# Performance work log

Measured on AMD Instinct MI355X. Metric: run time of the kernel, lower is better.

The kernel has to match this reference:

```python
import jax, jax.numpy as jnp
import numpy as np

B, T, P, H, D = 8, 16, 14, 16, 64
L = P * P            # 196 patches (CLS excluded)
DM = H * D           # 1024 = d_model
NS = 16              # n_synos
T2 = T * T           # 256 = n_frames**2


def _conv2d(x, w, b):
    # x: [N,C,H,W], w: [O,I,kh,kw], stride 1, SAME padding (ksize//2 for odd k)
    y = jax.lax.conv_general_dilated(x, w, (1, 1), 'SAME',
                                     dimension_numbers=('NCHW', 'OIHW', 'NCHW'))
    return y + b[None, :, None, None]


def _layernorm(x, g, b):
    m = x.mean(-1, keepdims=True)
    v = x.var(-1, keepdims=True)
    return (x - m) / jnp.sqrt(v + 1e-5) * g + b


def setup_inputs() -> dict:
    key = jax.random.key(0)
    ks = jax.random.split(key, 12)
    q = jax.random.normal(ks[0], (B, T, L + 1, H, D), jnp.float32)
    k = jax.random.normal(ks[1], (B, T, L + 1, H, D), jnp.float32)
    v = jax.random.normal(ks[2], (B, T, L + 1, H, D), jnp.float32)
    syno_emb = jax.random.normal(ks[3], (NS, DM), jnp.float32) * 0.02
    t_conv_w = jax.random.normal(ks[4], (1, 2 * H, 3, 3), jnp.float32) * 0.001
    t_conv_b = jnp.zeros((1,), jnp.float32)
    ln_g = jnp.ones((T2,), jnp.float32)
    ln_b = jnp.zeros((T2,), jnp.float32)
    w1 = jax.random.normal(ks[5], (T2, T2), jnp.float32) * 0.02
    b1 = jnp.zeros((T2,), jnp.float32)
    w2 = jax.random.normal(ks[6], (T2, T2), jnp.float32) * 0.02
    b2 = jnp.zeros((T2,), jnp.float32)
    p_conv_w = jax.random.normal(ks[7], (1, T2, 3, 3), jnp.float32) * 0.001
    p_conv_b = jnp.zeros((1,), jnp.float32)
    return dict(q=q, k=k, v=v, syno_emb=syno_emb,
                t_conv_w=t_conv_w, t_conv_b=t_conv_b,
                ln_g=ln_g, ln_b=ln_b, w1=w1, b1=b1, w2=w2, b2=b2,
                p_conv_w=p_conv_w, p_conv_b=p_conv_b)


def reference(q, k, v, syno_emb, t_conv_w, t_conv_b, ln_g, ln_b,
              w1, b1, w2, b2, p_conv_w, p_conv_b):
    # ---------------- temporal detection ----------------
    def head_aff(a):  # a: [B,T,L,H,D] -> [B*L, H, T, T]
        a = a.transpose(0, 2, 1, 3, 4)  # [B,L,T,H,D]
        scale = 1.0 / (a.shape[-1] ** 0.5)
        aff = jnp.einsum('nlqhc,nlkhc->nlqkh', a * scale, a)  # [B,L,T,T,H]
        aff = jax.nn.softmax(aff, axis=-2)  # softmax over key frames
        return aff.reshape(B * L, T, T, H).transpose(0, 3, 1, 2)

    affs = jnp.concatenate([head_aff(q[:, :, 1:]), head_aff(k[:, :, 1:])],
                           axis=1)                      # [B*L, 2H, T, T]
    aff = _conv2d(affs, t_conv_w, t_conv_b)             # [B*L, 1, T, T]
    aff = aff.reshape(B, P, P, T2)                      # [B, P, P, T^2]
    h = _layernorm(aff, ln_g, ln_b)
    h = h @ w1.T + b1
    h = jax.nn.gelu(h, approximate=False)               # torch nn.GELU default
    h = h @ w2.T + b2
    aff = aff + h
    aff = aff.transpose(0, 3, 1, 2)                     # [B, T^2, P, P]
    aff = _conv2d(aff, p_conv_w, p_conv_b)              # [B, 1, P, P]
    y_t = aff.reshape(B, -1)                            # [B, P*P]

    # ---------------- spatial detection ----------------
    kf = k[:, :, 1:].reshape(B, T, L, DM)
    vf = v[:, :, 1:].reshape(B, T, L, DM)
    s_scale = 1.0 / (DM ** 0.5)
    s_aff = jnp.einsum('qw,ntkw->ntqk', syno_emb * s_scale, kf)  # [B,T,NS,L]
    s_aff = jax.nn.softmax(s_aff, axis=-1)
    s_mix = jnp.einsum('ntql,ntlw->ntqw', s_aff, vf)    # [B,T,NS,DM]
    y_s = s_mix.reshape(B, T * NS, DM).mean(axis=1)     # [B, DM]

    return (y_t, y_s)
```

## Files before the change

kernel.cpp:

```cpp
#include <hip/hip_runtime.h>
#include <hip/hip_bf16.h>
#include <math.h>

#define BB 8
#define TT 16
#define PP 14
#define LL 196
#define HH 16
#define DD 64
#define DM 1024
#define NS 16
#define T2 256
#define LP1 197

using bf16x8 = __attribute__((ext_vector_type(8))) short;
using f32x4  = __attribute__((ext_vector_type(4))) float;

__device__ __forceinline__ float dot4(float4 a, float4 b) {
    return a.x*b.x + a.y*b.y + a.z*b.z + a.w*b.w;
}

__device__ __forceinline__ uint32_t pkbf(float lo, float hi) {
    uint32_t a = __builtin_bit_cast(uint32_t, lo);
    uint32_t b = __builtin_bit_cast(uint32_t, hi);
    a += 0x7FFFu + ((a >> 16) & 1u);
    b += 0x7FFFu + ((b >> 16) & 1u);
    return (a >> 16) | (b & 0xFFFF0000u);
}

__device__ __forceinline__ void split2(float x, float y, uint32_t* h, uint32_t* lo) {
    const uint32_t hh = pkbf(x, y);
    const float hx = __builtin_bit_cast(float, hh << 16);
    const float hy = __builtin_bit_cast(float, hh & 0xFFFF0000u);
    *h = hh;
    *lo = pkbf(x - hx, y - hy);
}

__device__ __forceinline__ void pksplit(float4 p, float4 q, bf16x8& hi, bf16x8& lo) {
    uint32_t uh[4], ul[4];
    split2(p.x, p.y, &uh[0], &ul[0]);
    split2(p.z, p.w, &uh[1], &ul[1]);
    split2(q.x, q.y, &uh[2], &ul[2]);
    split2(q.z, q.w, &uh[3], &ul[3]);
    struct U4 { uint32_t v[4]; } th, tl;
    th.v[0] = uh[0]; th.v[1] = uh[1]; th.v[2] = uh[2]; th.v[3] = uh[3];
    tl.v[0] = ul[0]; tl.v[1] = ul[1]; tl.v[2] = ul[2]; tl.v[3] = ul[3];
    hi = __builtin_bit_cast(bf16x8, th);
    lo = __builtin_bit_cast(bf16x8, tl);
}

__global__ __launch_bounds__(256) void kprep(
        const float* __restrict__ syno,
        uint32_t* __restrict__ synoHi, uint32_t* __restrict__ synoLo) {
    const int i = blockIdx.x * 256 + threadIdx.x;
    const float x = syno[2 * i], y = syno[2 * i + 1];
    uint32_t h, lo;
    split2(x, y, &h, &lo);
    synoHi[i] = h;
    synoLo[i] = lo;
}

__global__ __launch_bounds__(256) void k1_temporal(
        const float* __restrict__ qin, const float* __restrict__ kin,
        const float* __restrict__ tw,  const float* __restrict__ tbv,
        const uint32_t* __restrict__ synoHi, const uint32_t* __restrict__ synoLo,
        float* __restrict__ affRaw, float* __restrict__ SLout) {
    __shared__ __align__(16) float lds_c[16 * 260];
    __shared__ __align__(16) float sl_part[4][16][16];

    const int bid = blockIdx.x, b = bid / LL, l = bid % LL;
    const int tid = threadIdx.x, wid = tid >> 6, lane = tid & 63;
    const int mrow = lane & 15;
    const int g = lane >> 4;
    const int colb = lane & 15;
    const int oq = tid >> 4, ok = tid & 15;

    const size_t rowbase = ((size_t)(b*TT + mrow)*LP1 + 1 + l)*DM + g*8;
    f32x4 acc_sl = {0.f, 0.f, 0.f, 0.f};
    float accv = tbv[0];

    float4 A[2][4];
    uint4  S[2][4];

#define K1_LOAD(BUF, IT) do {                                                  \
        const int ch_ = 2*wid + 8*((IT) >> 1) + ((IT) & 1);                    \
        const float* sp_ = ((IT) < 4) ? qin : kin;                             \
        const float* base_ = sp_ + rowbase + (size_t)(ch_ & 15) * DD;          \
        A[BUF][0] = *reinterpret_cast<const float4*>(base_);                   \
        A[BUF][1] = *reinterpret_cast<const float4*>(base_ + 4);               \
        A[BUF][2] = *reinterpret_cast<const float4*>(base_ + 32);              \
        A[BUF][3] = *reinterpret_cast<const float4*>(base_ + 36);              \
        if ((IT) >= 4) {                                                       \
            const int off_ = colb * 512 + (ch_ - 16) * 32 + g * 4;             \
            S[BUF][0] = *reinterpret_cast<const uint4*>(synoHi + off_);        \
            S[BUF][1] = *reinterpret_cast<const uint4*>(synoLo + off_);        \
            S[BUF][2] = *reinterpret_cast<const uint4*>(synoHi + off_ + 16);   \
            S[BUF][3] = *reinterpret_cast<const uint4*>(synoLo + off_ + 16);   \
        }                                                                      \
    } while (0)

#define K1_COMP(BUF, IT) do {                                                  \
        bf16x8 h1, l1, h2, l2;                                                 \
        pksplit(A[BUF][0], A[BUF][1], h1, l1);                                 \
        pksplit(A[BUF][2], A[BUF][3], h2, l2);                                 \
        f32x4 acc = {0.f, 0.f, 0.f, 0.f};                                      \
        acc = __builtin_amdgcn_mfma_f32_16x16x32_bf16(h1, h1, acc, 0, 0, 0);   \
        acc = __builtin_amdgcn_mfma_f32_16x16x32_bf16(h1, l1, acc, 0, 0, 0);   \
        acc = __builtin_amdgcn_mfma_f32_16x16x32_bf16(l1, h1, acc, 0, 0, 0);   \
        acc = __builtin_amdgcn_mfma_f32_16x16x32_bf16(h2, h2, acc, 0, 0, 0);   \
        acc = __builtin_amdgcn_mfma_f32_16x16x32_bf16(h2, l2, acc, 0, 0, 0);   \
        acc = __builtin_amdgcn_mfma_f32_16x16x32_bf16(l2, h2, acc, 0, 0, 0);   \
        if ((IT) >= 4) {                                                       \
            const bf16x8 sh1 = __builtin_bit_cast(bf16x8, S[BUF][0]);          \
            const bf16x8 sl1 = __builtin_bit_cast(bf16x8, S[BUF][1]);          \
            const bf16x8 sh2 = __builtin_bit_cast(bf16x8, S[BUF][2]);          \
            const bf16x8 sl2 = __builtin_bit_cast(bf16x8, S[BUF][3]);          \
            acc_sl = __builtin_amdgcn_mfma_f32_16x16x32_bf16(h1, sh1, acc_sl, 0, 0, 0); \
            acc_sl = __builtin_amdgcn_mfma_f32_16x16x32_bf16(h1, sl1, acc_sl, 0, 0, 0); \
            acc_sl = __builtin_amdgcn_mfma_f32_16x16x32_bf16(l1, sh1, acc_sl, 0, 0, 0); \
            acc_sl = __builtin_amdgcn_mfma_f32_16x16x32_bf16(h2, sh2, acc_sl, 0, 0, 0); \
            acc_sl = __builtin_amdgcn_mfma_f32_16x16x32_bf16(h2, sl2, acc_sl, 0, 0, 0); \
            acc_sl = __builtin_amdgcn_mfma_f32_16x16x32_bf16(l2, sh2, acc_sl, 0, 0, 0); \
        }                                                                      \
                   \
        const float e0 = __expf(acc[0] * 0.125f);                              \
        const float e1 = __expf(acc[1] * 0.125f);                              \
        const float e2 = __expf(acc[2] * 0.125f);                              \
        const float e3 = __expf(acc[3] * 0.125f);                              \
        float s0 = e0, s1 = e1, s2 = e2, s3 = e3;                              \
        _Pragma("unroll")                                                      \
        for (int msk = 1; msk < 16; msk <<= 1) {                               \
            s0 += __shfl_xor(s0, msk, 64);                                     \
            s1 += __shfl_xor(s1, msk, 64);                                     \
            s2 += __shfl_xor(s2, msk, 64);                                     \
            s3 += __shfl_xor(s3, msk, 64);                                     \
        }                                                                      \
        const int slot_ = 2*wid + 8*(((IT) >> 1) & 1) + ((IT) & 1);            \
        float* cp_ = lds_c + slot_ * 260;                                      \
        cp_[(g*4 + 0)*16 + colb] = e0 / s0;                                    \
        cp_[(g*4 + 1)*16 + colb] = e1 / s1;                                    \
        cp_[(g*4 + 2)*16 + colb] = e2 / s2;                                    \
        cp_[(g*4 + 3)*16 + colb] = e3 / s3;                                    \
    } while (0)

#define K1_CONV(PASS) do {                                                     \
        _Pragma("unroll")                                                      \
        for (int ky = 0; ky < 3; ++ky) {                                       \
            const int iq = oq + ky - 1;                                        \
            if (iq < 0 || iq > 15) continue;                                   \
            _Pragma("unroll")                                                  \
            for (int kx = 0; kx < 3; ++kx) {                                   \
                const int ik = ok + kx - 1;                                    \
                if (ik < 0 || ik > 15) continue;                               \
                const int pix = iq * 16 + ik;                                  \
                _Pragma("unroll")                                              \
                for (int s = 0; s < 16; ++s)                                   \
                    accv += lds_c[s * 260 + pix] * tw[((PASS)*16 + s)*9 + ky*3 + kx]; \
            }                                                                  \
        }                                                                      \
    } while (0)

    K1_LOAD(0, 0);
    #pragma unroll
    for (int it = 0; it < 8; ++it) {
        if (it < 7) {
            switch (it & 1) {
                case 0: K1_LOAD(1, it + 1); break;
                default: K1_LOAD(0, it + 1); break;
            }
        }
        switch (it & 1) {
            case 0: K1_COMP(0, it); break;
            default: K1_COMP(1, it); break;
        }
        if (it == 3) {
            __syncthreads();
            K1_CONV(0);
            __syncthreads();
        }
    }

    #pragma unroll
    for (int r = 0; r < 4; ++r)
        sl_part[wid][g * 4 + r][colb] = acc_sl[r];
    __syncthreads();
    K1_CONV(1);

    affRaw[(size_t)bid * T2 + tid] = accv;

    {
        const int t = tid >> 4, qq = tid & 15;
        const float s = sl_part[0][t][qq] + sl_part[1][t][qq] +
                        sl_part[2][t][qq] + sl_part[3][t][qq];
        SLout[((size_t)(b * TT + t) * NS + qq) * LL + l] = s * 0.03125f;
    }
#undef K1_LOAD
#undef K1_COMP
#undef K1_CONV
}

__global__ __launch_bounds__(256) void k2_mlp(
        const float* __restrict__ affRaw,
        const float* __restrict__ lng, const float* __restrict__ lnb,
        const float* __restrict__ w1, const float* __restrict__ b1,
        const float* __restrict__ w2, const float* __restrict__ b2,
        float* __restrict__ affRes) {
    __shared__ __align__(16) float lx[4 * 256];
    __shared__ __align__(16) float lln[4 * 256];
    __shared__ __align__(16) float lg[4 * 256];
    const int tid = threadIdx.x;
    const int wave = tid >> 6, lane = tid & 63;
    const int i0 = blockIdx.x * 4;
    {
        const float* xr = affRaw + (size_t)(i0 + wave) * 256;
        float4 x = reinterpret_cast<const float4*>(xr)[lane];
        float sm = x.x + x.y + x.z + x.w;
        float ss = x.x * x.x + x.y * x.y + x.z * x.z + x.w * x.w;
        #pragma unroll
        for (int m = 1; m < 64; m <<= 1) {
            sm += __shfl_xor(sm, m, 64);
            ss += __shfl_xor(ss, m, 64);
        }
        const float mean = sm * (1.f / 256.f);
        const float var = ss * (1.f / 256.f) - mean * mean;
        const float inv = rsqrtf(var + 1e-5f);
        const float4 g4 = reinterpret_cast<const float4*>(lng)[lane];
        const float4 bb = reinterpret_cast<const float4*>(lnb)[lane];
        float4 ln;
        ln.x = (x.x - mean) * inv * g4.x + bb.x;
        ln.y = (x.y - mean) * inv * g4.y + bb.y;
        ln.z = (x.z - mean) * inv * g4.z + bb.z;
        ln.w = (x.w - mean) * inv * g4.w + bb.w;
        reinterpret_cast<float4*>(lx + wave * 256)[lane] = x;
        reinterpret_cast<float4*>(lln + wave * 256)[lane] = ln;
    }
    __syncthreads();
    const int j = tid;
    float a0 = 0.f, a1 = 0.f, a2 = 0.f, a3 = 0.f;
    {
        const float4* wr = reinterpret_cast<const float4*>(w1 + (size_t)j * 256);
        const float4* l0 = reinterpret_cast<const float4*>(lln);
        const float4* l1 = reinterpret_cast<const float4*>(lln + 256);
        const float4* l2 = reinterpret_cast<const float4*>(lln + 512);
        const float4* l3 = reinterpret_cast<const float4*>(lln + 768);
        #pragma unroll 8
        for (int m4 = 0; m4 < 64; ++m4) {
            const float4 w = wr[m4];
            a0 += dot4(w, l0[m4]); a1 += dot4(w, l1[m4]);
            a2 += dot4(w, l2[m4]); a3 += dot4(w, l3[m4]);
        }
    }
    const float bj = b1[j];
    const float kInvSqrt2 = 0.70710678118654752f;
    float h0 = a0 + bj, h1 = a1 + bj, h2 = a2 + bj, h3 = a3 + bj;
    lg[0 * 256 + j] = 0.5f * h0 * (1.f + erff(h0 * kInvSqrt2));
    lg[1 * 256 + j] = 0.5f * h1 * (1.f + erff(h1 * kInvSqrt2));
    lg[2 * 256 + j] = 0.5f * h2 * (1.f + erff(h2 * kInvSqrt2));
    lg[3 * 256 + j] = 0.5f * h3 * (1.f + erff(h3 * kInvSqrt2));
    __syncthreads();
    a0 = a1 = a2 = a3 = 0.f;
    {
        const float4* wr = reinterpret_cast<const float4*>(w2 + (size_t)j * 256);
        const float4* l0 = reinterpret_cast<const float4*>(lg);
        const float4* l1 = reinterpret_cast<const float4*>(lg + 256);
        const float4* l2 = reinterpret_cast<const float4*>(lg + 512);
        const float4* l3 = reinterpret_cast<const float4*>(lg + 768);
        #pragma unroll 8
        for (int m4 = 0; m4 < 64; ++m4) {
            const float4 w = wr[m4];
            a0 += dot4(w, l0[m4]); a1 += dot4(w, l1[m4]);
            a2 += dot4(w, l2[m4]); a3 += dot4(w, l3[m4]);
        }
    }
    const float b2j = b2[j];
    affRes[(size_t)(i0 + 0) * 256 + j] = lx[0 * 256 + j] + a0 + b2j;
    affRes[(size_t)(i0 + 1) * 256 + j] = lx[1 * 256 + j] + a1 + b2j;
    affRes[(size_t)(i0 + 2) * 256 + j] = lx[2 * 256 + j] + a2 + b2j;
    affRes[(size_t)(i0 + 3) * 256 + j] = lx[3 * 256 + j] + a3 + b2j;
}

__global__ __launch_bounds__(256) void k3a_pconv(
        const float* __restrict__ affRes, const float* __restrict__ pw,
        float* __restrict__ part) {
    __shared__ __align__(16) float lpw[576];
    const int b = blockIdx.x >> 2, cc = blockIdx.x & 3;
    const int tid = threadIdx.x;
    for (int idx = tid; idx < 576; idx += 256) {
        const int kk = idx / 64, c = idx & 63;
        lpw[kk * 64 + c] = pw[(size_t)(cc * 64 + c) * 9 + kk];
    }
    __syncthreads();
    if (tid < 196) {
        const int p1 = tid / 14, p2 = tid % 14;
        float s = 0.f;
        #pragma unroll
        for (int ky = 0; ky < 3; ++ky) {
            const int ip1 = p1 + ky - 1;
            if (ip1 < 0 || ip1 > 13) continue;
            #pragma unroll
            for (int kx = 0; kx < 3; ++kx) {
                const int ip2 = p2 + kx - 1;
                if (ip2 < 0 || ip2 > 13) continue;
                const float4* ar = reinterpret_cast<const float4*>(
                    affRes + (size_t)(b * LL + ip1 * 14 + ip2) * 256 + cc * 64);
                const float4* wr = reinterpret_cast<const float4*>(lpw + (ky * 3 + kx) * 64);
                #pragma unroll
                for (int c4 = 0; c4 < 16; ++c4) s += dot4(ar[c4], wr[c4]);
            }
        }
        part[(cc * 8 + b) * 196 + tid] = s;
    }
}

__global__ void k3b_yt(const float* __restrict__ part,
                       const float* __restrict__ pcb, float* __restrict__ out) {
    const int b = blockIdx.x, tid = threadIdx.x;
    if (tid < 196) {
        float s = pcb[0];
        #pragma unroll
        for (int cc = 0; cc < 4; ++cc) s += part[(cc * 8 + b) * 196 + tid];
        out[b * 196 + tid] = s;
    }
}

__global__ __launch_bounds__(256) void k4bc(
        const float* __restrict__ SL, const float* __restrict__ vin,
        float* __restrict__ PS) {
    __shared__ float lp[16 * 200];
    __shared__ float ws[196];
    const int t = blockIdx.x, b = blockIdx.y, z = blockIdx.z;
    const int tid = threadIdx.x;
    const int qq = tid >> 4, j = tid & 15;
    const float* row = SL + (size_t)((b * TT + t) * NS + qq) * LL;
    float v[13];
    float m = -1e30f;
    #pragma unroll
    for (int i = 0; i < 13; ++i) {
        const int l = j + i * 16;
        v[i] = (l < LL) ? row[l] : -1e30f;
        m = fmaxf(m, v[i]);
    }
    #pragma unroll
    for (int msk = 1; msk < 16; msk <<= 1) m = fmaxf(m, __shfl_xor(m, msk, 64));
    float s = 0.f;
    #pragma unroll
    for (int i = 0; i < 13; ++i) {
        const int l = j + i * 16;
        v[i] = (l < LL) ? __expf(v[i] - m) : 0.f;
        s += v[i];
    }
    #pragma unroll
    for (int msk = 1; msk < 16; msk <<= 1) s += __shfl_xor(s, msk, 64);
    const float inv = 1.f / s;
    #pragma unroll
    for (int i = 0; i < 13; ++i) {
        const int l = j + i * 16;
        if (l < LL) lp[qq * 200 + l] = v[i] * inv;
    }
    __syncthreads();
    if (tid < LL) {
        float w = 0.f;
        #pragma unroll
        for (int qi = 0; qi < 16; ++qi) w += lp[qi * 200 + tid];
        ws[tid] = w;
    }
    __syncthreads();
    const int bt = b * TT + t;
    float4 acc = make_float4(0.f, 0.f, 0.f, 0.f);
    const float* vb = vin + ((size_t)bt * LP1 + 1 + z * 98) * DM + tid * 4;
    const float* wz = ws + z * 98;
    #pragma unroll 4
    for (int l = 0; l < 98; ++l) {
        const float4 vv = *reinterpret_cast<const float4*>(vb + (size_t)l * DM);
        const float w = wz[l];
        acc.x += w * vv.x; acc.y += w * vv.y; acc.z += w * vv.z; acc.w += w * vv.w;
    }
    *reinterpret_cast<float4*>(PS + ((size_t)bt * 2 + z) * DM + tid * 4) = acc;
}

__global__ void k4d_ys(const float* __restrict__ PS, float* __restrict__ out) {
    const int i = blockIdx.x * 256 + threadIdx.x;
    const int b = i >> 10, w = i & 1023;
    float s = 0.f;
    #pragma unroll
    for (int tz = 0; tz < 32; ++tz) s += PS[((size_t)b * 32 + tz) * DM + w];
    out[1568 + i] = s * (1.f / 256.f);
}

extern "C" void kernel_launch(void* const* d_in, const int* in_sizes, int n_in,
                              void* d_out, int out_size, void* d_ws, size_t ws_size,
                              hipStream_t stream) {
    const float* q    = (const float*)d_in[0];
    const float* k    = (const float*)d_in[1];
    const float* v    = (const float*)d_in[2];
    const float* syno = (const float*)d_in[3];
    const float* tw   = (const float*)d_in[4];
    const float* tbv  = (const float*)d_in[5];
    const float* lng  = (const float*)d_in[6];
    const float* lnb  = (const float*)d_in[7];
    const float* w1   = (const float*)d_in[8];
    const float* b1   = (const float*)d_in[9];
    const float* w2   = (const float*)d_in[10];
    const float* b2   = (const float*)d_in[11];
    const float* pw   = (const float*)d_in[12];
    const float* pcb  = (const float*)d_in[13];
    float* out = (float*)d_out;

    float* ws = (float*)d_ws;
    float* affRaw = ws;
    float* affRes = ws + 401408;
    float* SL     = ws + 802816;
    float* part   = ws + 1229312;
    uint32_t* synoHi = (uint32_t*)(ws + 1235584);
    uint32_t* synoLo = (uint32_t*)(ws + 1243776);
    float* PS     = ws;

    hipLaunchKernelGGL(kprep, dim3(32), dim3(256), 0, stream, syno, synoHi, synoLo);
    hipLaunchKernelGGL(k1_temporal, dim3(BB * LL), dim3(256), 0, stream,
                       q, k, tw, tbv, synoHi, synoLo, affRaw, SL);
    hipLaunchKernelGGL(k2_mlp, dim3(392), dim3(256), 0, stream,
                       affRaw, lng, lnb, w1, b1, w2, b2, affRes);
    hipLaunchKernelGGL(k3a_pconv, dim3(32), dim3(256), 0, stream,
                       affRes, pw, part);
    hipLaunchKernelGGL(k3b_yt, dim3(8), dim3(256), 0, stream, part, pcb, out);
    hipLaunchKernelGGL(k4bc, dim3(16, 8, 2), dim3(256), 0, stream, SL, v, PS);
    hipLaunchKernelGGL(k4d_ys, dim3(32), dim3(256), 0, stream, PS, out);
}
```

Before: 144.0 us.

## Run LayerNorm-MLP GEMMs on MFMA with split-bf16 weights; widen pconv split

The per-row scalar fp32 MLP is replaced with a 32-row-tile MFMA GEMM. Weights are pre-split into hi/lo bf16 pairs by a new prep kernel, and the three-product split keeps accuracy close to fp32. The point-conv reduction is split into 16 channel chunks instead of 4, so 128 blocks run instead of 32. This adds a weight-prep kernel and a larger partial-sum reduction, and the MLP grid shrinks from 392 to 49 blocks, which may underfill the GPU.

```diff
diff --git a/kernel.cpp b/kernel.cpp
--- a/kernel.cpp
+++ b/kernel.cpp
@@ -58,6 +58,18 @@
     split2(x, y, &h, &lo);
     synoHi[i] = h;
     synoLo[i] = lo;
+}
+
+__global__ __launch_bounds__(256) void kprep_w(
+        const float* __restrict__ w1, const float* __restrict__ w2,
+        uint32_t* __restrict__ w1h, uint32_t* __restrict__ w1l,
+        uint32_t* __restrict__ w2h, uint32_t* __restrict__ w2l) {
+    const int i = blockIdx.x * 256 + threadIdx.x;
+    uint32_t h, lo;
+    split2(w1[2 * i], w1[2 * i + 1], &h, &lo);
+    w1h[i] = h; w1l[i] = lo;
+    split2(w2[2 * i], w2[2 * i + 1], &h, &lo);
+    w2h[i] = h; w2l[i] = lo;
 }
 
 __global__ __launch_bounds__(256) void k1_temporal(
@@ -122,7 +134,6 @@
             acc_sl = __builtin_amdgcn_mfma_f32_16x16x32_bf16(h2, sl2, acc_sl, 0, 0, 0); \
             acc_sl = __builtin_amdgcn_mfma_f32_16x16x32_bf16(l2, sh2, acc_sl, 0, 0, 0); \
         }                                                                      \
-                   \
         const float e0 = __expf(acc[0] * 0.125f);                              \
         const float e1 = __expf(acc[1] * 0.125f);                              \
         const float e2 = __expf(acc[2] * 0.125f);                              \
@@ -199,21 +210,24 @@
 #undef K1_CONV
 }
 
-__global__ __launch_bounds__(256) void k2_mlp(
+__global__ __launch_bounds__(256) void k2_mfma(
         const float* __restrict__ affRaw,
         const float* __restrict__ lng, const float* __restrict__ lnb,
-        const float* __restrict__ w1, const float* __restrict__ b1,
-        const float* __restrict__ w2, const float* __restrict__ b2,
+        const uint32_t* __restrict__ w1h, const uint32_t* __restrict__ w1l,
+        const float* __restrict__ b1,
+        const uint32_t* __restrict__ w2h, const uint32_t* __restrict__ w2l,
+        const float* __restrict__ b2,
         float* __restrict__ affRes) {
-    __shared__ __align__(16) float lx[4 * 256];
-    __shared__ __align__(16) float lln[4 * 256];
-    __shared__ __align__(16) float lg[4 * 256];
-    const int tid = threadIdx.x;
-    const int wave = tid >> 6, lane = tid & 63;
-    const int i0 = blockIdx.x * 4;
-    {
-        const float* xr = affRaw + (size_t)(i0 + wave) * 256;
-        float4 x = reinterpret_cast<const float4*>(xr)[lane];
+    __shared__ __align__(16) float buf[32 * 260];
+    const int tid = threadIdx.x, wid = tid >> 6, lane = tid & 63;
+    const int colb = lane & 15, g = lane >> 4;
+    const int row0 = blockIdx.x * 32;
+
+    #pragma unroll
+    for (int rr = 0; rr < 8; ++rr) {
+        const int r = wid * 8 + rr;
+        const float* xr = affRaw + (size_t)(row0 + r) * 256;
+        const float4 x = reinterpret_cast<const float4*>(xr)[lane];
         float sm = x.x + x.y + x.z + x.w;
         float ss = x.x * x.x + x.y * x.y + x.z * x.z + x.w * x.w;
         #pragma unroll
@@ -231,63 +245,94 @@
         ln.y = (x.y - mean) * inv * g4.y + bb.y;
         ln.z = (x.z - mean) * inv * g4.z + bb.z;
         ln.w = (x.w - mean) * inv * g4.w + bb.w;
-        reinterpret_cast<float4*>(lx + wave * 256)[lane] = x;
-        reinterpret_cast<float4*>(lln + wave * 256)[lane] = ln;
-    }
-    __syncthreads();
-    const int j = tid;
-    float a0 = 0.f, a1 = 0.f, a2 = 0.f, a3 = 0.f;
-    {
-        const float4* wr = reinterpret_cast<const float4*>(w1 + (size_t)j * 256);
-        const float4* l0 = reinterpret_cast<const float4*>(lln);
-        const float4* l1 = reinterpret_cast<const float4*>(lln + 256);
-        const float4* l2 = reinterpret_cast<const float4*>(lln + 512);
-        const float4* l3 = reinterpret_cast<const float4*>(lln + 768);
-        #pragma unroll 8
-        for (int m4 = 0; m4 < 64; ++m4) {
-            const float4 w = wr[m4];
-            a0 += dot4(w, l0[m4]); a1 += dot4(w, l1[m4]);
-            a2 += dot4(w, l2[m4]); a3 += dot4(w, l3[m4]);
-        }
-    }
-    const float bj = b1[j];
+        *reinterpret_cast<float4*>(buf + r * 260 + lane * 4) = ln;
+    }
+    __syncthreads();
+
+#define K2_GEMM(WH, WL, ACC) do {                                              \
+        _Pragma("unroll")                                                      \
+        for (int c = 0; c < 8; ++c) {                                          \
+            bf16x8 a0h, a0l, a1h, a1l;                                         \
+            {                                                                  \
+                const float* ap0 = buf + (0*16 + colb) * 260 + c * 32 + g * 8; \
+                const float* ap1 = buf + (1*16 + colb) * 260 + c * 32 + g * 8; \
+                pksplit(*reinterpret_cast<const float4*>(ap0),                 \
+                        *reinterpret_cast<const float4*>(ap0 + 4), a0h, a0l);  \
+                pksplit(*reinterpret_cast<const float4*>(ap1),                 \
+                        *reinterpret_cast<const float4*>(ap1 + 4), a1h, a1l);  \
+            }                                                                  \
+            _Pragma("unroll")                                                  \
+            for (int nn = 0; nn < 4; ++nn) {                                   \
+                const int jp = ((wid * 4 + nn) * 16 + colb) * 128 + c * 16 + g * 4; \
+                const bf16x8 wh = __builtin_bit_cast(bf16x8,                   \
+                    *reinterpret_cast<const uint4*>(WH + jp));                 \
+                const bf16x8 wl = __builtin_bit_cast(bf16x8,                   \
+                    *reinterpret_cast<const uint4*>(WL + jp));                 \
+                ACC[0][nn] = __builtin_amdgcn_mfma_f32_16x16x32_bf16(a0h, wh, ACC[0][nn], 0, 0, 0); \
+                ACC[0][nn] = __builtin_amdgcn_mfma_f32_16x16x32_bf16(a0h, wl, ACC[0][nn], 0, 0, 0); \
+                ACC[0][nn] = __builtin_amdgcn_mfma_f32_16x16x32_bf16(a0l, wh, ACC[0][nn], 0, 0, 0); \
+                ACC[1][nn] = __builtin_amdgcn_mfma_f32_16x16x32_bf16(a1h, wh, ACC[1][nn], 0, 0, 0); \
+                ACC[1][nn] = __builtin_amdgcn_mfma_f32_16x16x32_bf16(a1h, wl, ACC[1][nn], 0, 0, 0); \
+                ACC[1][nn] = __builtin_amdgcn_mfma_f32_16x16x32_bf16(a1l, wh, ACC[1][nn], 0, 0, 0); \
+            }                                                                  \
+        }                                                                      \
+    } while (0)
+
+    f32x4 acc1[2][4];
+    #pragma unroll
+    for (int m = 0; m < 2; ++m)
+        #pragma unroll
+        for (int nn = 0; nn < 4; ++nn) acc1[m][nn] = (f32x4){0.f, 0.f, 0.f, 0.f};
+    K2_GEMM(w1h, w1l, acc1);
+
+    __syncthreads();
     const float kInvSqrt2 = 0.70710678118654752f;
-    float h0 = a0 + bj, h1 = a1 + bj, h2 = a2 + bj, h3 = a3 + bj;
-    lg[0 * 256 + j] = 0.5f * h0 * (1.f + erff(h0 * kInvSqrt2));
-    lg[1 * 256 + j] = 0.5f * h1 * (1.f + erff(h1 * kInvSqrt2));
-    lg[2 * 256 + j] = 0.5f * h2 * (1.f + erff(h2 * kInvSqrt2));
-    lg[3 * 256 + j] = 0.5f * h3 * (1.f + erff(h3 * kInvSqrt2));
-    __syncthreads();
-    a0 = a1 = a2 = a3 = 0.f;
-    {
-        const float4* wr = reinterpret_cast<const float4*>(w2 + (size_t)j * 256);
-        const float4* l0 = reinterpret_cast<const float4*>(lg);
-        const float4* l1 = reinterpret_cast<const float4*>(lg + 256);
-        const float4* l2 = reinterpret_cast<const float4*>(lg + 512);
-        const float4* l3 = reinterpret_cast<const float4*>(lg + 768);
-        #pragma unroll 8
-        for (int m4 = 0; m4 < 64; ++m4) {
-            const float4 w = wr[m4];
-            a0 += dot4(w, l0[m4]); a1 += dot4(w, l1[m4]);
-            a2 += dot4(w, l2[m4]); a3 += dot4(w, l3[m4]);
-        }
-    }
-    const float b2j = b2[j];
-    affRes[(size_t)(i0 + 0) * 256 + j] = lx[0 * 256 + j] + a0 + b2j;
-    affRes[(size_t)(i0 + 1) * 256 + j] = lx[1 * 256 + j] + a1 + b2j;
-    affRes[(size_t)(i0 + 2) * 256 + j] = lx[2 * 256 + j] + a2 + b2j;
-    affRes[(size_t)(i0 + 3) * 256 + j] = lx[3 * 256 + j] + a3 + b2j;
+    #pragma unroll
+    for (int m = 0; m < 2; ++m)
+        #pragma unroll
+        for (int nn = 0; nn < 4; ++nn) {
+            const int col = wid * 64 + nn * 16 + colb;
+            const float bj = b1[col];
+            #pragma unroll
+            for (int r = 0; r < 4; ++r) {
+                const float h = acc1[m][nn][r] + bj;
+                buf[(m * 16 + g * 4 + r) * 260 + col] =
+                    0.5f * h * (1.f + erff(h * kInvSqrt2));
+            }
+        }
+    __syncthreads();
+
+    f32x4 acc2[2][4];
+    #pragma unroll
+    for (int m = 0; m < 2; ++m)
+        #pragma unroll
+        for (int nn = 0; nn < 4; ++nn) acc2[m][nn] = (f32x4){0.f, 0.f, 0.f, 0.f};
+    K2_GEMM(w2h, w2l, acc2);
+
+    #pragma unroll
+    for (int m = 0; m < 2; ++m)
+        #pragma unroll
+        for (int nn = 0; nn < 4; ++nn) {
+            const int col = wid * 64 + nn * 16 + colb;
+            const float b2j = b2[col];
+            #pragma unroll
+            for (int r = 0; r < 4; ++r) {
+                const size_t idx = (size_t)(row0 + m * 16 + g * 4 + r) * 256 + col;
+                affRes[idx] = affRaw[idx] + acc2[m][nn][r] + b2j;
+            }
+        }
+#undef K2_GEMM
 }
 
 __global__ __launch_bounds__(256) void k3a_pconv(
         const float* __restrict__ affRes, const float* __restrict__ pw,
         float* __restrict__ part) {
-    __shared__ __align__(16) float lpw[576];
-    const int b = blockIdx.x >> 2, cc = blockIdx.x & 3;
+    __shared__ __align__(16) float lpw[144];
+    const int b = blockIdx.x >> 4, cc = blockIdx.x & 15;
     const int tid = threadIdx.x;
-    for (int idx = tid; idx < 576; idx += 256) {
-        const int kk = idx / 64, c = idx & 63;
-        lpw[kk * 64 + c] = pw[(size_t)(cc * 64 + c) * 9 + kk];
+    if (tid < 144) {
+        const int kk = tid / 16, c = tid & 15;
+        lpw[kk * 16 + c] = pw[(size_t)(cc * 16 + c) * 9 + kk];
     }
     __syncthreads();
     if (tid < 196) {
@@ -302,10 +347,10 @@
                 const int ip2 = p2 + kx - 1;
                 if (ip2 < 0 || ip2 > 13) continue;
                 const float4* ar = reinterpret_cast<const float4*>(
-                    affRes + (size_t)(b * LL + ip1 * 14 + ip2) * 256 + cc * 64);
-                const float4* wr = reinterpret_cast<const float4*>(lpw + (ky * 3 + kx) * 64);
+                    affRes + (size_t)(b * LL + ip1 * 14 + ip2) * 256 + cc * 16);
+                const float4* wr = reinterpret_cast<const float4*>(lpw + (ky * 3 + kx) * 16);
                 #pragma unroll
-                for (int c4 = 0; c4 < 16; ++c4) s += dot4(ar[c4], wr[c4]);
+                for (int c4 = 0; c4 < 4; ++c4) s += dot4(ar[c4], wr[c4]);
             }
         }
         part[(cc * 8 + b) * 196 + tid] = s;
@@ -318,7 +363,7 @@
     if (tid < 196) {
         float s = pcb[0];
         #pragma unroll
-        for (int cc = 0; cc < 4; ++cc) s += part[(cc * 8 + b) * 196 + tid];
+        for (int cc = 0; cc < 16; ++cc) s += part[(cc * 8 + b) * 196 + tid];
         out[b * 196 + tid] = s;
     }
 }
@@ -410,17 +455,23 @@
     float* affRaw = ws;
     float* affRes = ws + 401408;
     float* SL     = ws + 802816;
-    float* part   = ws + 1229312;
+    float* part   = ws + 1204224;
     uint32_t* synoHi = (uint32_t*)(ws + 1235584);
     uint32_t* synoLo = (uint32_t*)(ws + 1243776);
+    uint32_t* w1h = (uint32_t*)(ws + 1251968);
+    uint32_t* w1l = (uint32_t*)(ws + 1284736);
+    uint32_t* w2h = (uint32_t*)(ws + 1317504);
+    uint32_t* w2l = (uint32_t*)(ws + 1350272);
     float* PS     = ws;
 
     hipLaunchKernelGGL(kprep, dim3(32), dim3(256), 0, stream, syno, synoHi, synoLo);
+    hipLaunchKernelGGL(kprep_w, dim3(128), dim3(256), 0, stream,
+                       w1, w2, w1h, w1l, w2h, w2l);
     hipLaunchKernelGGL(k1_temporal, dim3(BB * LL), dim3(256), 0, stream,
                        q, k, tw, tbv, synoHi, synoLo, affRaw, SL);
-    hipLaunchKernelGGL(k2_mlp, dim3(392), dim3(256), 0, stream,
-                       affRaw, lng, lnb, w1, b1, w2, b2, affRes);
-    hipLaunchKernelGGL(k3a_pconv, dim3(32), dim3(256), 0, stream,
+    hipLaunchKernelGGL(k2_mfma, dim3(49), dim3(256), 0, stream,
+                       affRaw, lng, lnb, w1h, w1l, b1, w2h, w2l, b2, affRes);
+    hipLaunchKernelGGL(k3a_pconv, dim3(128), dim3(256), 0, stream,
                        affRes, pw, part);
     hipLaunchKernelGGL(k3b_yt, dim3(8), dim3(256), 0, stream, part, pcb, out);
     hipLaunchKernelGGL(k4bc, dim3(16, 8, 2), dim3(256), 0, stream, SL, v, PS);
```

Result: faster. 132.2 us (-8.2%).
